# Performance work log

Measured on AMD Instinct MI355X. Metric: run time of the kernel, lower is better.

## Reference

```python
import jax, jax.numpy as jnp
import numpy as np

ALPHA = 1.702   # swiglu_alpha
LIMIT = 7.0     # swiglu_limit
EPS = 1e-5      # norm_eps
E = 16          # num_experts
K = 4           # experts_per_token


def _swiglu(h):
    # interleaved split as in torch: even cols -> glu, odd cols -> linear
    x_glu = jnp.minimum(h[..., ::2], LIMIT)
    # faithful to source bug: clamp(min=limit, max=limit) == constant limit
    x_lin = jnp.clip(h[..., 1::2], LIMIT, LIMIT)
    return x_glu * jax.nn.sigmoid(ALPHA * x_glu) * (x_lin + 1.0)


def setup_inputs() -> dict:
    key = jax.random.key(0)
    ks = jax.random.split(key, 7)
    B, T, H, I = 1, 2048, 1024, 1024
    x = jax.random.normal(ks[0], (B, T, H), jnp.float32)
    scale = jnp.ones((H,), jnp.float32)
    gate_w = jax.random.normal(ks[1], (E, H), jnp.float32) * 0.02
    gate_b = jnp.zeros((E,), jnp.float32)
    mlp1_w = jax.random.normal(ks[2], (E, 2 * I, H), jnp.float32) * 0.02
    mlp1_b = jax.random.normal(ks[3], (E, 2 * I), jnp.float32) * 0.02
    mlp2_w = jax.random.normal(ks[4], (E, H, I), jnp.float32) * 0.02
    mlp2_b = jax.random.normal(ks[5], (E, H), jnp.float32) * 0.02
    return dict(x=x, scale=scale, gate_w=gate_w, gate_b=gate_b,
                mlp1_w=mlp1_w, mlp1_b=mlp1_b, mlp2_w=mlp2_w, mlp2_b=mlp2_b)


def reference(x, scale, gate_w, gate_b, mlp1_w, mlp1_b, mlp2_w, mlp2_b):
    # RMSNorm (fp32 math, identity cast here since inputs are fp32)
    t = x * jax.lax.rsqrt(jnp.mean(x * x, axis=-1, keepdims=True) + EPS) * scale
    # gate + top-k routing (sorted descending, matching torch.topk sorted=True)
    g = jnp.einsum('bth,eh->bte', t, gate_w) + gate_b          # [B,T,E]
    vals, idx = jax.lax.top_k(g, K)                            # [B,T,K]
    w = jax.nn.softmax(vals, axis=-1)                          # [B,T,K]
    # route[b,t,e] = sum_k w[b,t,k] * [idx[b,t,k]==e]  (top-k indices distinct)
    route = jnp.sum(jax.nn.one_hot(idx, E, dtype=t.dtype) * w[..., None], axis=-2)
    route_e = jnp.moveaxis(route, -1, 0)                       # [E,B,T]
    # grouped dense-per-expert computation instead of per-token weight gather:
    # mathematically identical output, avoids materializing [B,T,K,2I,H] gathers
    def step(acc, p):
        w1, b1, w2, b2, r = p
        h = jnp.einsum('bth,ih->bti', t, w1) + b1              # [B,T,2I]
        s = _swiglu(h)                                         # [B,T,I]
        y = jnp.einsum('bti,hi->bth', s, w2) + b2              # [B,T,H]
        return acc + r[..., None] * y, None
    acc, _ = jax.lax.scan(step, jnp.zeros_like(x),
                          (mlp1_w, mlp1_b, mlp2_w, mlp2_b, route_e))
    return x + acc
```

## Files before the change

kernel.cpp:

```cpp
#include <hip/hip_runtime.h>
#include <hip/hip_bf16.h>

typedef __bf16 bf16;
typedef __bf16 bf16x4 __attribute__((ext_vector_type(4)));
typedef __bf16 bf16x8 __attribute__((ext_vector_type(8)));
typedef float f32x4 __attribute__((ext_vector_type(4)));

constexpr int TKN  = 2048;
constexpr int HD   = 1024;
constexpr int NEXP = 16;
constexpr int KSEL = 4;
constexpr int IDIM = 1024;
constexpr int I2   = 2048;
constexpr int NROW = TKN * KSEL;

__device__ __forceinline__ void async_copy16(const void* g, void* l) {
  __builtin_amdgcn_global_load_lds((__attribute__((address_space(1))) void*)g,
                                   (__attribute__((address_space(3))) void*)l,
                                   16, 0, 0);
}

__global__ __launch_bounds__(256) void k_norm_gate(
    const float* __restrict__ x, const float* __restrict__ scale,
    const float* __restrict__ gate_w, const float* __restrict__ gate_b,
    float* __restrict__ out, bf16* __restrict__ tN,
    int* __restrict__ eids, float* __restrict__ wts)
{
  __shared__ float tLds[HD];
  __shared__ float red[4];
  __shared__ float gsh[NEXP];
  const int tid = threadIdx.x;
  const int tok = blockIdx.x;
  const int wid = tid >> 6, lane = tid & 63;

  const float4 x4 = *(const float4*)(x + (size_t)tok * HD + tid * 4);
  float ss = x4.x * x4.x + x4.y * x4.y + x4.z * x4.z + x4.w * x4.w;
  #pragma unroll
  for (int off = 32; off > 0; off >>= 1) ss += __shfl_down(ss, off);
  if (lane == 0) red[wid] = ss;
  __syncthreads();
  ss = red[0] + red[1] + red[2] + red[3];
  const float r = rsqrtf(ss * (1.0f / HD) + 1e-5f);

  const float4 s4 = *(const float4*)(scale + tid * 4);
  float4 t4;
  t4.x = x4.x * r * s4.x; t4.y = x4.y * r * s4.y;
  t4.z = x4.z * r * s4.z; t4.w = x4.w * r * s4.w;
  *(float4*)(out + (size_t)tok * HD + tid * 4) = x4;
  tLds[tid * 4 + 0] = t4.x; tLds[tid * 4 + 1] = t4.y;
  tLds[tid * 4 + 2] = t4.z; tLds[tid * 4 + 3] = t4.w;
  bf16x4 tb;
  tb[0] = (bf16)t4.x; tb[1] = (bf16)t4.y; tb[2] = (bf16)t4.z; tb[3] = (bf16)t4.w;
  *(bf16x4*)(tN + (size_t)tok * HD + tid * 4) = tb;
  __syncthreads();

  {
    const int e = tid >> 4, l16 = tid & 15;
    float p = 0.f;
    const float* gw = gate_w + (size_t)e * HD;
    for (int j = l16; j < HD; j += 16) p += tLds[j] * gw[j];
    p += __shfl_xor(p, 8); p += __shfl_xor(p, 4);
    p += __shfl_xor(p, 2); p += __shfl_xor(p, 1);
    if (l16 == 0) gsh[e] = p + gate_b[e];
  }
  __syncthreads();

  if (tid == 0) {
    float g[NEXP];
    #pragma unroll
    for (int i = 0; i < NEXP; ++i) g[i] = gsh[i];
    int   bi[KSEL]; float bv[KSEL];
    #pragma unroll
    for (int k = 0; k < KSEL; ++k) {
      float best = -1e30f; int b = 0;
      for (int i = 0; i < NEXP; ++i) if (g[i] > best) { best = g[i]; b = i; }
      bv[k] = best; bi[k] = b; g[b] = -1e30f;
    }
    const float m = bv[0];
    float wv[KSEL], sum = 0.f;
    #pragma unroll
    for (int k = 0; k < KSEL; ++k) { wv[k] = __expf(bv[k] - m); sum += wv[k]; }
    const float inv = 1.0f / sum;
    #pragma unroll
    for (int k = 0; k < KSEL; ++k) {
      eids[tok * KSEL + k] = bi[k];
      wts[tok * KSEL + k]  = wv[k] * inv;
    }
  }
}

__global__ __launch_bounds__(256) void k_route(
    const int* __restrict__ eids, const float* __restrict__ wts,
    int* __restrict__ cntg, int* __restrict__ segg,
    int* __restrict__ rowTok, float* __restrict__ rowW)
{
  __shared__ int hcnt[NEXP], hoff[NEXP], hrun[NEXP];
  const int tid = threadIdx.x;
  if (tid < NEXP) { hcnt[tid] = 0; hrun[tid] = 0; }
  __syncthreads();
  for (int i = tid; i < NROW; i += 256) atomicAdd(&hcnt[eids[i]], 1);
  __syncthreads();
  if (tid == 0) {
    int s = 0;
    for (int e = 0; e < NEXP; ++e) { hoff[e] = s; segg[e] = s; cntg[e] = hcnt[e]; s += hcnt[e]; }
  }
  __syncthreads();
  for (int i = tid; i < NROW; i += 256) {
    const int e = eids[i];
    const int slot = atomicAdd(&hrun[e], 1);
    const int row = hoff[e] + slot;
    rowTok[row] = i >> 2;
    rowW[row]   = wts[i];
  }
}

__global__ __launch_bounds__(256) void k_cvt_w1(const float* __restrict__ w1,
                                                bf16* __restrict__ w1b) {
  const size_t f = (size_t)blockIdx.x * 256 + threadIdx.x;
  const size_t row = f >> 7;
  const int    off = (int)(f & 127) * 8;
  const size_t e = row >> 10, n = row & 1023;
  const float* s = w1 + (e * 2048 + 2 * n) * 1024 + off;
  const float4 a = *(const float4*)(s);
  const float4 b = *(const float4*)(s + 4);
  bf16x8 o;
  o[0] = (bf16)a.x; o[1] = (bf16)a.y; o[2] = (bf16)a.z; o[3] = (bf16)a.w;
  o[4] = (bf16)b.x; o[5] = (bf16)b.y; o[6] = (bf16)b.z; o[7] = (bf16)b.w;
  *(bf16x8*)(w1b + row * 1024 + off) = o;
}

__global__ __launch_bounds__(256) void k_cvt_w2(const float* __restrict__ w2,
                                                bf16* __restrict__ w2b) {
  const size_t f = (size_t)blockIdx.x * 256 + threadIdx.x;
  const size_t base = f * 8;
  const float4 a = *(const float4*)(w2 + base);
  const float4 b = *(const float4*)(w2 + base + 4);
  bf16x8 o;
  o[0] = (bf16)a.x; o[1] = (bf16)a.y; o[2] = (bf16)a.z; o[3] = (bf16)a.w;
  o[4] = (bf16)b.x; o[5] = (bf16)b.y; o[6] = (bf16)b.z; o[7] = (bf16)b.w;
  *(bf16x8*)(w2b + base) = o;
}

template <bool PREP>
__global__ __launch_bounds__(256) void k_gemm1(
    const bf16* __restrict__ tN, const float* __restrict__ w1,
    const bf16* __restrict__ w1b, const float* __restrict__ b1,
    const int* __restrict__ cnt, const int* __restrict__ segOff,
    const int* __restrict__ rowTok, bf16* __restrict__ sBuf)
{
  const int e = blockIdx.z, mt = blockIdx.y, nt = blockIdx.x;
  const int rows = cnt[e];
  if (mt * 128 >= rows) return;
  const int soff = segOff[e];
  __shared__ __align__(16) bf16 Asm[128 * 32];
  __shared__ __align__(16) bf16 Bsm[128 * 32];
  const int tid = threadIdx.x;
  const int wid = tid >> 6, lane = tid & 63;
  const int quad = lane >> 4, l16 = lane & 15;
  const int wm = wid & 1, wn = wid >> 1;

  const int r0 = wid * 16 + (lane >> 2);
  const int r1 = 64 + r0;
  const int colE = (lane & 3) * 8;
  const int m0 = min(mt * 128 + r0, rows - 1);
  const int m1 = min(mt * 128 + r1, rows - 1);
  const char* gA0 = (const char*)(tN + (size_t)rowTok[soff + m0] * HD + colE);
  const char* gA1 = (const char*)(tN + (size_t)rowTok[soff + m1] * HD + colE);
  bf16* lA0 = Asm + wid * 512;
  bf16* lA1 = Asm + 2048 + wid * 512;

  const int n0 = nt * 128;
  const char* gB0 = (const char*)(w1b + (size_t)e * IDIM * HD + (size_t)(n0 + r0) * HD + colE);
  const char* gB1 = (const char*)(w1b + (size_t)e * IDIM * HD + (size_t)(n0 + r1) * HD + colE);
  bf16* lB0 = Bsm + wid * 512;
  bf16* lB1 = Bsm + 2048 + wid * 512;
  const int brow = tid >> 3;
  const int bkk  = (tid & 7) * 4;
  const float* gB = w1 + (size_t)e * I2 * HD + (size_t)(2 * (n0 + brow)) * HD + bkk;

  const f32x4 zero = {0.f, 0.f, 0.f, 0.f};
  f32x4 acc[4][4];
  #pragma unroll
  for (int i = 0; i < 4; ++i)
    #pragma unroll
    for (int j = 0; j < 4; ++j) acc[i][j] = zero;

  for (int kt = 0; kt < 32; ++kt) {
    async_copy16(gA0, lA0);
    async_copy16(gA1, lA1);
    gA0 += 64; gA1 += 64;
    if constexpr (PREP) {
      async_copy16(gB0, lB0);
      async_copy16(gB1, lB1);
      gB0 += 64; gB1 += 64;
    } else {
      #pragma unroll
      for (int q = 0; q < 4; ++q) {
        const float4 v = *(const float4*)(gB + (size_t)q * 64 * HD);
        bf16x4 c;
        c[0] = (bf16)v.x; c[1] = (bf16)v.y; c[2] = (bf16)v.z; c[3] = (bf16)v.w;
        *(bf16x4*)(Bsm + (q * 32 + brow) * 32 + bkk) = c;
      }
      gB += 32;
    }
    __syncthreads();
    bf16x8 av[4], bv[4];
    #pragma unroll
    for (int i = 0; i < 4; ++i)
      av[i] = *(const bf16x8*)(Asm + (wm * 64 + i * 16 + l16) * 32 + quad * 8);
    #pragma unroll
    for (int j = 0; j < 4; ++j)
      bv[j] = *(const bf16x8*)(Bsm + (wn * 64 + j * 16 + l16) * 32 + quad * 8);
    #pragma unroll
    for (int i = 0; i < 4; ++i)
      #pragma unroll
      for (int j = 0; j < 4; ++j)
        acc[i][j] = __builtin_amdgcn_mfma_f32_16x16x32_bf16(av[i], bv[j], acc[i][j], 0, 0, 0);
    __syncthreads();
  }

  const int mbase = mt * 128 + wm * 64;
  #pragma unroll
  for (int j = 0; j < 4; ++j) {
    const int ncol = n0 + wn * 64 + j * 16 + l16;
    const float bias = b1[(size_t)e * I2 + 2 * ncol];
    #pragma unroll
    for (int i = 0; i < 4; ++i) {
      #pragma unroll
      for (int rg = 0; rg < 4; ++rg) {
        const int gm = mbase + i * 16 + quad * 4 + rg;
        if (gm < rows) {
          const float h  = acc[i][j][rg] + bias;
          const float xg = fminf(h, 7.0f);
          const float s  = xg * (1.0f / (1.0f + __expf(-1.702f * xg))) * 8.0f;
          sBuf[((size_t)soff + gm) * IDIM + ncol] = (bf16)s;
        }
      }
    }
  }
}

template <bool PREP>
__global__ __launch_bounds__(256) void k_gemm2(
    const bf16* __restrict__ sBuf, const float* __restrict__ w2,
    const bf16* __restrict__ w2b, const float* __restrict__ b2,
    const int* __restrict__ cnt, const int* __restrict__ segOff,
    const int* __restrict__ rowTok, const float* __restrict__ rowW,
    float* __restrict__ out)
{
  const int e = blockIdx.z, mt = blockIdx.y, nt = blockIdx.x;
  const int rows = cnt[e];
  if (mt * 128 >= rows) return;
  const int soff = segOff[e];
  __shared__ __align__(16) bf16 Asm[128 * 32];
  __shared__ __align__(16) bf16 Bsm[128 * 32];
  const int tid = threadIdx.x;
  const int wid = tid >> 6, lane = tid & 63;
  const int quad = lane >> 4, l16 = lane & 15;
  const int wm = wid & 1, wn = wid >> 1;

  const int r0 = wid * 16 + (lane >> 2);
  const int r1 = 64 + r0;
  const int colE = (lane & 3) * 8;
  const int m0 = min(mt * 128 + r0, rows - 1);
  const int m1 = min(mt * 128 + r1, rows - 1);
  const char* gA0 = (const char*)(sBuf + ((size_t)soff + m0) * IDIM + colE);
  const char* gA1 = (const char*)(sBuf + ((size_t)soff + m1) * IDIM + colE);
  bf16* lA0 = Asm + wid * 512;
  bf16* lA1 = Asm + 2048 + wid * 512;

  const int n0 = nt * 128;
  const char* gB0 = (const char*)(w2b + (size_t)e * HD * IDIM + (size_t)(n0 + r0) * IDIM + colE);
  const char* gB1 = (const char*)(w2b + (size_t)e * HD * IDIM + (size_t)(n0 + r1) * IDIM + colE);
  bf16* lB0 = Bsm + wid * 512;
  bf16* lB1 = Bsm + 2048 + wid * 512;
  const int brow = tid >> 3;
  const int bkk  = (tid & 7) * 4;
  const float* gB = w2 + (size_t)e * HD * IDIM + (size_t)(n0 + brow) * IDIM + bkk;

  const f32x4 zero = {0.f, 0.f, 0.f, 0.f};
  f32x4 acc[4][4];
  #pragma unroll
  for (int i = 0; i < 4; ++i)
    #pragma unroll
    for (int j = 0; j < 4; ++j) acc[i][j] = zero;

  for (int kt = 0; kt < 32; ++kt) {
    async_copy16(gA0, lA0);
    async_copy16(gA1, lA1);
    gA0 += 64; gA1 += 64;
    if constexpr (PREP) {
      async_copy16(gB0, lB0);
      async_copy16(gB1, lB1);
      gB0 += 64; gB1 += 64;
    } else {
      #pragma unroll
      for (int q = 0; q < 4; ++q) {
        const float4 v = *(const float4*)(gB + (size_t)q * 32 * IDIM);
        bf16x4 c;
        c[0] = (bf16)v.x; c[1] = (bf16)v.y; c[2] = (bf16)v.z; c[3] = (bf16)v.w;
        *(bf16x4*)(Bsm + (q * 32 + brow) * 32 + bkk) = c;
      }
      gB += 32;
    }
    __syncthreads();
    bf16x8 av[4], bv[4];
    #pragma unroll
    for (int i = 0; i < 4; ++i)
      av[i] = *(const bf16x8*)(Asm + (wm * 64 + i * 16 + l16) * 32 + quad * 8);
    #pragma unroll
    for (int j = 0; j < 4; ++j)
      bv[j] = *(const bf16x8*)(Bsm + (wn * 64 + j * 16 + l16) * 32 + quad * 8);
    #pragma unroll
    for (int i = 0; i < 4; ++i)
      #pragma unroll
      for (int j = 0; j < 4; ++j)
        acc[i][j] = __builtin_amdgcn_mfma_f32_16x16x32_bf16(av[i], bv[j], acc[i][j], 0, 0, 0);
    __syncthreads();
  }

  const int mbase = mt * 128 + wm * 64;
  #pragma unroll
  for (int j = 0; j < 4; ++j) {
    const int ncol = n0 + wn * 64 + j * 16 + l16;
    const float bias = b2[(size_t)e * HD + ncol];
    #pragma unroll
    for (int i = 0; i < 4; ++i) {
      #pragma unroll
      for (int rg = 0; rg < 4; ++rg) {
        const int gm = mbase + i * 16 + quad * 4 + rg;
        if (gm < rows) {
          const int   tok = rowTok[soff + gm];
          const float wgt = rowW[soff + gm];
          atomicAdd(out + (size_t)tok * HD + ncol, wgt * (acc[i][j][rg] + bias));
        }
      }
    }
  }
}

extern "C" void kernel_launch(void* const* d_in, const int* in_sizes, int n_in,
                              void* d_out, int out_size, void* d_ws, size_t ws_size,
                              hipStream_t stream) {
  const float* x      = (const float*)d_in[0];
  const float* scale  = (const float*)d_in[1];
  const float* gate_w = (const float*)d_in[2];
  const float* gate_b = (const float*)d_in[3];
  const float* w1     = (const float*)d_in[4];
  const float* b1     = (const float*)d_in[5];
  const float* w2     = (const float*)d_in[6];
  const float* b2     = (const float*)d_in[7];
  float* out = (float*)d_out;

  char* p = (char*)d_ws;
  bf16* tN   = (bf16*)p;  p += (size_t)TKN * HD * 2;
  bf16* sBuf = (bf16*)p;  p += (size_t)NROW * IDIM * 2;
  int*   eids   = (int*)p;   p += (size_t)NROW * 4;
  float* wts    = (float*)p; p += (size_t)NROW * 4;
  int*   rowTok = (int*)p;   p += (size_t)NROW * 4;
  float* rowW   = (float*)p; p += (size_t)NROW * 4;
  int*   cntg   = (int*)p;   p += 256;
  int*   segg   = (int*)p;   p += 256;
  const size_t base_need = (size_t)(p - (char*)d_ws);
  const size_t WSZ = (size_t)NEXP * IDIM * HD * 2;
  bf16* w2b = (bf16*)p;
  bf16* w1b = (bf16*)(p + WSZ);
  const bool prep2 = ws_size >= base_need + WSZ;
  const bool prep1 = ws_size >= base_need + 2 * WSZ;

  k_norm_gate<<<TKN, 256, 0, stream>>>(x, scale, gate_w, gate_b, out, tN, eids, wts);
  k_route<<<1, 256, 0, stream>>>(eids, wts, cntg, segg, rowTok, rowW);
  if (prep1) k_cvt_w1<<<8192, 256, 0, stream>>>(w1, w1b);
  if (prep2) k_cvt_w2<<<8192, 256, 0, stream>>>(w2, w2b);

  if (prep1)
    k_gemm1<true><<<dim3(8, 16, NEXP), 256, 0, stream>>>(tN, w1, w1b, b1, cntg, segg, rowTok, sBuf);
  else
    k_gemm1<false><<<dim3(8, 16, NEXP), 256, 0, stream>>>(tN, w1, w1b, b1, cntg, segg, rowTok, sBuf);

  if (prep2)
    k_gemm2<true><<<dim3(8, 16, NEXP), 256, 0, stream>>>(sBuf, w2, w2b, b2, cntg, segg, rowTok, rowW, out);
  else
    k_gemm2<false><<<dim3(8, 16, NEXP), 256, 0, stream>>>(sBuf, w2, w2b, b2, cntg, segg, rowTok, rowW, out);
}
```

Measured before the change: 387.8 us.

## Retile expert GEMMs to 64-row tiles, deepen K step, and replace atomics with finalize

```diff
diff --git a/kernel.cpp b/kernel.cpp
--- a/kernel.cpp
+++ b/kernel.cpp
@@ -92,7 +92,7 @@
 __global__ __launch_bounds__(256) void k_route(
     const int* __restrict__ eids, const float* __restrict__ wts,
     int* __restrict__ cntg, int* __restrict__ segg,
-    int* __restrict__ rowTok, float* __restrict__ rowW)
+    int* __restrict__ rowTok, float* __restrict__ rowW, int* __restrict__ rowOf)
 {
   __shared__ int hcnt[NEXP], hoff[NEXP], hrun[NEXP];
   const int tid = threadIdx.x;
@@ -111,42 +111,233 @@
     const int row = hoff[e] + slot;
     rowTok[row] = i >> 2;
     rowW[row]   = wts[i];
-  }
-}
-
-__global__ __launch_bounds__(256) void k_cvt_w1(const float* __restrict__ w1,
-                                                bf16* __restrict__ w1b) {
-  const size_t f = (size_t)blockIdx.x * 256 + threadIdx.x;
-  const size_t row = f >> 7;
-  const int    off = (int)(f & 127) * 8;
-  const size_t e = row >> 10, n = row & 1023;
-  const float* s = w1 + (e * 2048 + 2 * n) * 1024 + off;
-  const float4 a = *(const float4*)(s);
-  const float4 b = *(const float4*)(s + 4);
-  bf16x8 o;
-  o[0] = (bf16)a.x; o[1] = (bf16)a.y; o[2] = (bf16)a.z; o[3] = (bf16)a.w;
-  o[4] = (bf16)b.x; o[5] = (bf16)b.y; o[6] = (bf16)b.z; o[7] = (bf16)b.w;
-  *(bf16x8*)(w1b + row * 1024 + off) = o;
-}
-
-__global__ __launch_bounds__(256) void k_cvt_w2(const float* __restrict__ w2,
-                                                bf16* __restrict__ w2b) {
-  const size_t f = (size_t)blockIdx.x * 256 + threadIdx.x;
-  const size_t base = f * 8;
-  const float4 a = *(const float4*)(w2 + base);
-  const float4 b = *(const float4*)(w2 + base + 4);
-  bf16x8 o;
-  o[0] = (bf16)a.x; o[1] = (bf16)a.y; o[2] = (bf16)a.z; o[3] = (bf16)a.w;
-  o[4] = (bf16)b.x; o[5] = (bf16)b.y; o[6] = (bf16)b.z; o[7] = (bf16)b.w;
-  *(bf16x8*)(w2b + base) = o;
-}
-
-template <bool PREP>
-__global__ __launch_bounds__(256) void k_gemm1(
+    rowOf[i]    = row;
+  }
+}
+
+__global__ __launch_bounds__(256) void k_cvt_all(const float* __restrict__ w1,
+                                                 const float* __restrict__ w2,
+                                                 bf16* __restrict__ w1b,
+                                                 bf16* __restrict__ w2b) {
+  const size_t bid = blockIdx.x;
+  if (bid < 8192) {
+    const size_t f = bid * 256 + threadIdx.x;
+    const size_t row = f >> 7;
+    const int    off = (int)(f & 127) * 8;
+    const size_t e = row >> 10, n = row & 1023;
+    const float* s = w1 + (e * 2048 + 2 * n) * 1024 + off;
+    const float4 a = *(const float4*)(s);
+    const float4 b = *(const float4*)(s + 4);
+    bf16x8 o;
+    o[0] = (bf16)a.x; o[1] = (bf16)a.y; o[2] = (bf16)a.z; o[3] = (bf16)a.w;
+    o[4] = (bf16)b.x; o[5] = (bf16)b.y; o[6] = (bf16)b.z; o[7] = (bf16)b.w;
+    *(bf16x8*)(w1b + row * 1024 + off) = o;
+  } else {
+    const size_t f = (bid - 8192) * 256 + threadIdx.x;
+    const size_t base = f * 8;
+    const float4 a = *(const float4*)(w2 + base);
+    const float4 b = *(const float4*)(w2 + base + 4);
+    bf16x8 o;
+    o[0] = (bf16)a.x; o[1] = (bf16)a.y; o[2] = (bf16)a.z; o[3] = (bf16)a.w;
+    o[4] = (bf16)b.x; o[5] = (bf16)b.y; o[6] = (bf16)b.z; o[7] = (bf16)b.w;
+    *(bf16x8*)(w2b + base) = o;
+  }
+}
+
+
+__global__ __launch_bounds__(256) void k_gemm1v2(
+    const bf16* __restrict__ tN, const bf16* __restrict__ w1b,
+    const float* __restrict__ b1, const int* __restrict__ cnt,
+    const int* __restrict__ segOff, const int* __restrict__ rowTok,
+    bf16* __restrict__ sBuf)
+{
+  const int e = blockIdx.z, mt = blockIdx.y, nt = blockIdx.x;
+  const int rows = cnt[e];
+  if (mt * 64 >= rows) return;
+  const int soff = segOff[e];
+  __shared__ __align__(16) bf16 Asm[2 * 64 * 32];
+  __shared__ __align__(16) bf16 Bsm[2 * 128 * 32];
+  const int tid = threadIdx.x;
+  const int wid = tid >> 6, lane = tid & 63;
+  const int quad = lane >> 4, l16 = lane & 15;
+  const int wm = wid & 1, wn = wid >> 1;
+
+  const int r0 = wid * 16 + (lane >> 2);
+  const int colE = (lane & 3) * 8;
+  const int mA = min(mt * 64 + r0, rows - 1);
+  const char* gA  = (const char*)(tN + (size_t)rowTok[soff + mA] * HD + colE);
+  const int n0 = nt * 128;
+  const char* gB0 = (const char*)(w1b + ((size_t)e * IDIM + n0 + r0) * HD + colE);
+  const char* gB1 = (const char*)(w1b + ((size_t)e * IDIM + n0 + 64 + r0) * HD + colE);
+  bf16* lA  = Asm + wid * 512;
+  bf16* lB0 = Bsm + wid * 512;
+  bf16* lB1 = Bsm + 2048 + wid * 512;
+
+  const f32x4 zero = {0.f, 0.f, 0.f, 0.f};
+  f32x4 acc[2][4];
+  #pragma unroll
+  for (int i = 0; i < 2; ++i)
+    #pragma unroll
+    for (int j = 0; j < 4; ++j) acc[i][j] = zero;
+
+  for (int kt = 0; kt < 16; ++kt) {
+    async_copy16(gA, lA);
+    async_copy16(gB0, lB0);
+    async_copy16(gB1, lB1);
+    async_copy16(gA + 64, lA + 2048);
+    async_copy16(gB0 + 64, lB0 + 4096);
+    async_copy16(gB1 + 64, lB1 + 4096);
+    gA += 128; gB0 += 128; gB1 += 128;
+    __syncthreads();
+    bf16x8 av[2];
+    #pragma unroll
+    for (int s = 0; s < 2; ++s) {
+      av[0] = *(const bf16x8*)(Asm + s * 2048 + (wm * 32 + 0 * 16 + l16) * 32 + quad * 8);
+      av[1] = *(const bf16x8*)(Asm + s * 2048 + (wm * 32 + 1 * 16 + l16) * 32 + quad * 8);
+      #pragma unroll
+      for (int j = 0; j < 4; ++j) {
+        const bf16x8 bv = *(const bf16x8*)(Bsm + s * 4096 + (wn * 64 + j * 16 + l16) * 32 + quad * 8);
+        acc[0][j] = __builtin_amdgcn_mfma_f32_16x16x32_bf16(av[0], bv, acc[0][j], 0, 0, 0);
+        acc[1][j] = __builtin_amdgcn_mfma_f32_16x16x32_bf16(av[1], bv, acc[1][j], 0, 0, 0);
+      }
+    }
+    __syncthreads();
+  }
+
+  const int mbase = mt * 64 + wm * 32;
+  #pragma unroll
+  for (int j = 0; j < 4; ++j) {
+    const int ncol = n0 + wn * 64 + j * 16 + l16;
+    const float bias = b1[(size_t)e * I2 + 2 * ncol];
+    #pragma unroll
+    for (int i = 0; i < 2; ++i) {
+      #pragma unroll
+      for (int rg = 0; rg < 4; ++rg) {
+        const int gm = mbase + i * 16 + quad * 4 + rg;
+        if (gm < rows) {
+          const float h  = acc[i][j][rg] + bias;
+          const float xg = fminf(h, 7.0f);
+          const float s  = xg * (1.0f / (1.0f + __expf(-1.702f * xg))) * 8.0f;
+          sBuf[((size_t)soff + gm) * IDIM + ncol] = (bf16)s;
+        }
+      }
+    }
+  }
+}
+
+template <bool USEY>
+__global__ __launch_bounds__(256) void k_gemm2v2(
+    const bf16* __restrict__ sBuf, const bf16* __restrict__ w2b,
+    const float* __restrict__ b2, const int* __restrict__ cnt,
+    const int* __restrict__ segOff, const int* __restrict__ rowTok,
+    const float* __restrict__ rowW, bf16* __restrict__ yBuf,
+    float* __restrict__ out)
+{
+  const int e = blockIdx.z, mt = blockIdx.y, nt = blockIdx.x;
+  const int rows = cnt[e];
+  if (mt * 64 >= rows) return;
+  const int soff = segOff[e];
+  __shared__ __align__(16) bf16 Asm[2 * 64 * 32];
+  __shared__ __align__(16) bf16 Bsm[2 * 128 * 32];
+  const int tid = threadIdx.x;
+  const int wid = tid >> 6, lane = tid & 63;
+  const int quad = lane >> 4, l16 = lane & 15;
+  const int wm = wid & 1, wn = wid >> 1;
+
+  const int r0 = wid * 16 + (lane >> 2);
+  const int colE = (lane & 3) * 8;
+  const int mA = min(mt * 64 + r0, rows - 1);
+  const char* gA  = (const char*)(sBuf + ((size_t)soff + mA) * IDIM + colE);
+  const int n0 = nt * 128;
+  const char* gB0 = (const char*)(w2b + ((size_t)e * HD + n0 + r0) * IDIM + colE);
+  const char* gB1 = (const char*)(w2b + ((size_t)e * HD + n0 + 64 + r0) * IDIM + colE);
+  bf16* lA  = Asm + wid * 512;
+  bf16* lB0 = Bsm + wid * 512;
+  bf16* lB1 = Bsm + 2048 + wid * 512;
+
+  const f32x4 zero = {0.f, 0.f, 0.f, 0.f};
+  f32x4 acc[2][4];
+  #pragma unroll
+  for (int i = 0; i < 2; ++i)
+    #pragma unroll
+    for (int j = 0; j < 4; ++j) acc[i][j] = zero;
+
+  for (int kt = 0; kt < 16; ++kt) {
+    async_copy16(gA, lA);
+    async_copy16(gB0, lB0);
+    async_copy16(gB1, lB1);
+    async_copy16(gA + 64, lA + 2048);
+    async_copy16(gB0 + 64, lB0 + 4096);
+    async_copy16(gB1 + 64, lB1 + 4096);
+    gA += 128; gB0 += 128; gB1 += 128;
+    __syncthreads();
+    bf16x8 av[2];
+    #pragma unroll
+    for (int s = 0; s < 2; ++s) {
+      av[0] = *(const bf16x8*)(Asm + s * 2048 + (wm * 32 + 0 * 16 + l16) * 32 + quad * 8);
+      av[1] = *(const bf16x8*)(Asm + s * 2048 + (wm * 32 + 1 * 16 + l16) * 32 + quad * 8);
+      #pragma unroll
+      for (int j = 0; j < 4; ++j) {
+        const bf16x8 bv = *(const bf16x8*)(Bsm + s * 4096 + (wn * 64 + j * 16 + l16) * 32 + quad * 8);
+        acc[0][j] = __builtin_amdgcn_mfma_f32_16x16x32_bf16(av[0], bv, acc[0][j], 0, 0, 0);
+        acc[1][j] = __builtin_amdgcn_mfma_f32_16x16x32_bf16(av[1], bv, acc[1][j], 0, 0, 0);
+      }
+    }
+    __syncthreads();
+  }
+
+  const int mbase = mt * 64 + wm * 32;
+  #pragma unroll
+  for (int j = 0; j < 4; ++j) {
+    const int ncol = n0 + wn * 64 + j * 16 + l16;
+    const float bias = b2[(size_t)e * HD + ncol];
+    #pragma unroll
+    for (int i = 0; i < 2; ++i) {
+      #pragma unroll
+      for (int rg = 0; rg < 4; ++rg) {
+        const int gm = mbase + i * 16 + quad * 4 + rg;
+        if (gm < rows) {
+          if constexpr (USEY) {
+            yBuf[((size_t)soff + gm) * HD + ncol] = (bf16)(acc[i][j][rg] + bias);
+          } else {
+            atomicAdd(out + (size_t)rowTok[soff + gm] * HD + ncol,
+                      rowW[soff + gm] * (acc[i][j][rg] + bias));
+          }
+        }
+      }
+    }
+  }
+}
+
+__global__ __launch_bounds__(256) void k_finalize(
+    const float* __restrict__ x, const bf16* __restrict__ yBuf,
+    const int* __restrict__ rowOf, const float* __restrict__ wts,
+    float* __restrict__ out)
+{
+  const int tok = blockIdx.x;
+  const int tid = threadIdx.x;
+  const int r0 = rowOf[tok * 4 + 0], r1 = rowOf[tok * 4 + 1];
+  const int r2 = rowOf[tok * 4 + 2], r3 = rowOf[tok * 4 + 3];
+  const float w0 = wts[tok * 4 + 0], w1 = wts[tok * 4 + 1];
+  const float w2 = wts[tok * 4 + 2], w3 = wts[tok * 4 + 3];
+  const int col = tid * 4;
+  float4 o = *(const float4*)(x + (size_t)tok * HD + col);
+  const bf16x4 y0 = *(const bf16x4*)(yBuf + (size_t)r0 * HD + col);
+  const bf16x4 y1 = *(const bf16x4*)(yBuf + (size_t)r1 * HD + col);
+  const bf16x4 y2 = *(const bf16x4*)(yBuf + (size_t)r2 * HD + col);
+  const bf16x4 y3 = *(const bf16x4*)(yBuf + (size_t)r3 * HD + col);
+  o.x += w0 * (float)y0[0] + w1 * (float)y1[0] + w2 * (float)y2[0] + w3 * (float)y3[0];
+  o.y += w0 * (float)y0[1] + w1 * (float)y1[1] + w2 * (float)y2[1] + w3 * (float)y3[1];
+  o.z += w0 * (float)y0[2] + w1 * (float)y1[2] + w2 * (float)y2[2] + w3 * (float)y3[2];
+  o.w += w0 * (float)y0[3] + w1 * (float)y1[3] + w2 * (float)y2[3] + w3 * (float)y3[3];
+  *(float4*)(out + (size_t)tok * HD + col) = o;
+}
+
+__global__ __launch_bounds__(256) void k_gemm1_fb(
     const bf16* __restrict__ tN, const float* __restrict__ w1,
-    const bf16* __restrict__ w1b, const float* __restrict__ b1,
-    const int* __restrict__ cnt, const int* __restrict__ segOff,
-    const int* __restrict__ rowTok, bf16* __restrict__ sBuf)
+    const float* __restrict__ b1, const int* __restrict__ cnt,
+    const int* __restrict__ segOff, const int* __restrict__ rowTok,
+    bf16* __restrict__ sBuf)
 {
   const int e = blockIdx.z, mt = blockIdx.y, nt = blockIdx.x;
   const int rows = cnt[e];
@@ -158,7 +349,6 @@
   const int wid = tid >> 6, lane = tid & 63;
   const int quad = lane >> 4, l16 = lane & 15;
   const int wm = wid & 1, wn = wid >> 1;
-
   const int r0 = wid * 16 + (lane >> 2);
   const int r1 = 64 + r0;
   const int colE = (lane & 3) * 8;
@@ -168,14 +358,9 @@
   const char* gA1 = (const char*)(tN + (size_t)rowTok[soff + m1] * HD + colE);
   bf16* lA0 = Asm + wid * 512;
   bf16* lA1 = Asm + 2048 + wid * 512;
-
-  const int n0 = nt * 128;
-  const char* gB0 = (const char*)(w1b + (size_t)e * IDIM * HD + (size_t)(n0 + r0) * HD + colE);
-  const char* gB1 = (const char*)(w1b + (size_t)e * IDIM * HD + (size_t)(n0 + r1) * HD + colE);
-  bf16* lB0 = Bsm + wid * 512;
-  bf16* lB1 = Bsm + 2048 + wid * 512;
   const int brow = tid >> 3;
   const int bkk  = (tid & 7) * 4;
+  const int n0 = nt * 128;
   const float* gB = w1 + (size_t)e * I2 * HD + (size_t)(2 * (n0 + brow)) * HD + bkk;
 
   const f32x4 zero = {0.f, 0.f, 0.f, 0.f};
@@ -189,20 +374,14 @@
     async_copy16(gA0, lA0);
     async_copy16(gA1, lA1);
     gA0 += 64; gA1 += 64;
-    if constexpr (PREP) {
-      async_copy16(gB0, lB0);
-      async_copy16(gB1, lB1);
-      gB0 += 64; gB1 += 64;
-    } else {
-      #pragma unroll
-      for (int q = 0; q < 4; ++q) {
-        const float4 v = *(const float4*)(gB + (size_t)q * 64 * HD);
-        bf16x4 c;
-        c[0] = (bf16)v.x; c[1] = (bf16)v.y; c[2] = (bf16)v.z; c[3] = (bf16)v.w;
-        *(bf16x4*)(Bsm + (q * 32 + brow) * 32 + bkk) = c;
-      }
-      gB += 32;
-    }
+    #pragma unroll
+    for (int q = 0; q < 4; ++q) {
+      const float4 v = *(const float4*)(gB + (size_t)q * 64 * HD);
+      bf16x4 c;
+      c[0] = (bf16)v.x; c[1] = (bf16)v.y; c[2] = (bf16)v.z; c[3] = (bf16)v.w;
+      *(bf16x4*)(Bsm + (q * 32 + brow) * 32 + bkk) = c;
+    }
+    gB += 32;
     __syncthreads();
     bf16x8 av[4], bv[4];
     #pragma unroll
@@ -218,7 +397,6 @@
         acc[i][j] = __builtin_amdgcn_mfma_f32_16x16x32_bf16(av[i], bv[j], acc[i][j], 0, 0, 0);
     __syncthreads();
   }
-
   const int mbase = mt * 128 + wm * 64;
   #pragma unroll
   for (int j = 0; j < 4; ++j) {
@@ -240,13 +418,11 @@
   }
 }
 
-template <bool PREP>
-__global__ __launch_bounds__(256) void k_gemm2(
+__global__ __launch_bounds__(256) void k_gemm2_fb(
     const bf16* __restrict__ sBuf, const float* __restrict__ w2,
-    const bf16* __restrict__ w2b, const float* __restrict__ b2,
-    const int* __restrict__ cnt, const int* __restrict__ segOff,
-    const int* __restrict__ rowTok, const float* __restrict__ rowW,
-    float* __restrict__ out)
+    const float* __restrict__ b2, const int* __restrict__ cnt,
+    const int* __restrict__ segOff, const int* __restrict__ rowTok,
+    const float* __restrict__ rowW, float* __restrict__ out)
 {
   const int e = blockIdx.z, mt = blockIdx.y, nt = blockIdx.x;
   const int rows = cnt[e];
@@ -258,7 +434,6 @@
   const int wid = tid >> 6, lane = tid & 63;
   const int quad = lane >> 4, l16 = lane & 15;
   const int wm = wid & 1, wn = wid >> 1;
-
   const int r0 = wid * 16 + (lane >> 2);
   const int r1 = 64 + r0;
   const int colE = (lane & 3) * 8;
@@ -268,14 +443,9 @@
   const char* gA1 = (const char*)(sBuf + ((size_t)soff + m1) * IDIM + colE);
   bf16* lA0 = Asm + wid * 512;
   bf16* lA1 = Asm + 2048 + wid * 512;
-
-  const int n0 = nt * 128;
-  const char* gB0 = (const char*)(w2b + (size_t)e * HD * IDIM + (size_t)(n0 + r0) * IDIM + colE);
-  const char* gB1 = (const char*)(w2b + (size_t)e * HD * IDIM + (size_t)(n0 + r1) * IDIM + colE);
-  bf16* lB0 = Bsm + wid * 512;
-  bf16* lB1 = Bsm + 2048 + wid * 512;
   const int brow = tid >> 3;
   const int bkk  = (tid & 7) * 4;
+  const int n0 = nt * 128;
   const float* gB = w2 + (size_t)e * HD * IDIM + (size_t)(n0 + brow) * IDIM + bkk;
 
   const f32x4 zero = {0.f, 0.f, 0.f, 0.f};
@@ -289,20 +459,14 @@
     async_copy16(gA0, lA0);
     async_copy16(gA1, lA1);
     gA0 += 64; gA1 += 64;
-    if constexpr (PREP) {
-      async_copy16(gB0, lB0);
-      async_copy16(gB1, lB1);
-      gB0 += 64; gB1 += 64;
-    } else {
-      #pragma unroll
-      for (int q = 0; q < 4; ++q) {
-        const float4 v = *(const float4*)(gB + (size_t)q * 32 * IDIM);
-        bf16x4 c;
-        c[0] = (bf16)v.x; c[1] = (bf16)v.y; c[2] = (bf16)v.z; c[3] = (bf16)v.w;
-        *(bf16x4*)(Bsm + (q * 32 + brow) * 32 + bkk) = c;
-      }
-      gB += 32;
-    }
+    #pragma unroll
+    for (int q = 0; q < 4; ++q) {
+      const float4 v = *(const float4*)(gB + (size_t)q * 32 * IDIM);
+      bf16x4 c;
+      c[0] = (bf16)v.x; c[1] = (bf16)v.y; c[2] = (bf16)v.z; c[3] = (bf16)v.w;
+      *(bf16x4*)(Bsm + (q * 32 + brow) * 32 + bkk) = c;
+    }
+    gB += 32;
     __syncthreads();
     bf16x8 av[4], bv[4];
     #pragma unroll
@@ -318,7 +482,6 @@
         acc[i][j] = __builtin_amdgcn_mfma_f32_16x16x32_bf16(av[i], bv[j], acc[i][j], 0, 0, 0);
     __syncthreads();
   }
-
   const int mbase = mt * 128 + wm * 64;
   #pragma unroll
   for (int j = 0; j < 4; ++j) {
@@ -330,9 +493,8 @@
       for (int rg = 0; rg < 4; ++rg) {
         const int gm = mbase + i * 16 + quad * 4 + rg;
         if (gm < rows) {
-          const int   tok = rowTok[soff + gm];
-          const float wgt = rowW[soff + gm];
-          atomicAdd(out + (size_t)tok * HD + ncol, wgt * (acc[i][j][rg] + bias));
+          atomicAdd(out + (size_t)rowTok[soff + gm] * HD + ncol,
+                    rowW[soff + gm] * (acc[i][j][rg] + bias));
         }
       }
     }
@@ -359,27 +521,38 @@
   float* wts    = (float*)p; p += (size_t)NROW * 4;
   int*   rowTok = (int*)p;   p += (size_t)NROW * 4;
   float* rowW   = (float*)p; p += (size_t)NROW * 4;
+  int*   rowOf  = (int*)p;   p += (size_t)NROW * 4;
   int*   cntg   = (int*)p;   p += 256;
   int*   segg   = (int*)p;   p += 256;
   const size_t base_need = (size_t)(p - (char*)d_ws);
   const size_t WSZ = (size_t)NEXP * IDIM * HD * 2;
-  bf16* w2b = (bf16*)p;
-  bf16* w1b = (bf16*)(p + WSZ);
+  bf16* w2b  = (bf16*)p;
+  bf16* w1b  = (bf16*)(p + WSZ);
+  bf16* yBuf = (bf16*)(p + 2 * WSZ);
   const bool prep2 = ws_size >= base_need + WSZ;
   const bool prep1 = ws_size >= base_need + 2 * WSZ;
+  const bool useY  = prep1 && prep2 &&
+                     (ws_size >= base_need + 2 * WSZ + (size_t)NROW * HD * 2);
 
   k_norm_gate<<<TKN, 256, 0, stream>>>(x, scale, gate_w, gate_b, out, tN, eids, wts);
-  k_route<<<1, 256, 0, stream>>>(eids, wts, cntg, segg, rowTok, rowW);
-  if (prep1) k_cvt_w1<<<8192, 256, 0, stream>>>(w1, w1b);
-  if (prep2) k_cvt_w2<<<8192, 256, 0, stream>>>(w2, w2b);
-
-  if (prep1)
-    k_gemm1<true><<<dim3(8, 16, NEXP), 256, 0, stream>>>(tN, w1, w1b, b1, cntg, segg, rowTok, sBuf);
-  else
-    k_gemm1<false><<<dim3(8, 16, NEXP), 256, 0, stream>>>(tN, w1, w1b, b1, cntg, segg, rowTok, sBuf);
-
-  if (prep2)
-    k_gemm2<true><<<dim3(8, 16, NEXP), 256, 0, stream>>>(sBuf, w2, w2b, b2, cntg, segg, rowTok, rowW, out);
-  else
-    k_gemm2<false><<<dim3(8, 16, NEXP), 256, 0, stream>>>(sBuf, w2, w2b, b2, cntg, segg, rowTok, rowW, out);
-}
+  k_route<<<1, 256, 0, stream>>>(eids, wts, cntg, segg, rowTok, rowW, rowOf);
+
+  if (prep1 && prep2) {
+    k_cvt_all<<<16384, 256, 0, stream>>>(w1, w2, w1b, w2b);
+  }
+
+  if (prep1 && prep2) {
+    k_gemm1v2<<<dim3(8, 32, NEXP), 256, 0, stream>>>(tN, w1b, b1, cntg, segg, rowTok, sBuf);
+    if (useY) {
+      k_gemm2v2<true><<<dim3(8, 32, NEXP), 256, 0, stream>>>(sBuf, w2b, b2, cntg, segg,
+                                                             rowTok, rowW, yBuf, out);
+      k_finalize<<<TKN, 256, 0, stream>>>(x, yBuf, rowOf, wts, out);
+    } else {
+      k_gemm2v2<false><<<dim3(8, 32, NEXP), 256, 0, stream>>>(sBuf, w2b, b2, cntg, segg,
+                                                              rowTok, rowW, yBuf, out);
+    }
+  } else {
+    k_gemm1_fb<<<dim3(8, 16, NEXP), 256, 0, stream>>>(tN, w1, b1, cntg, segg, rowTok, sBuf);
+    k_gemm2_fb<<<dim3(8, 16, NEXP), 256, 0, stream>>>(sBuf, w2, b2, cntg, segg, rowTok, rowW, out);
+  }
+}
```

Result: faster. 380.1 us (-2.0%).
